# Optimization experiments

Measured on AMD Instinct MI355X. Metric: run time of the kernel, lower is better.

Reference implementation:

```python
import math
import jax, jax.numpy as jnp
import numpy as np

STREAMS = 4
DIM = 1024
M = 16                      # routing granularity
BUS = STREAMS * DIM         # 4096
C = BUS // M                # 256
SINK_ITERS = 10
SINK_TAU = 0.05
B, L = 4, 2048


def rms_norm(x, gamma):
    # F.normalize(x, dim=-1) * sqrt(dim) * (gamma + 1)
    norm = jnp.sqrt(jnp.sum(x * x, axis=-1, keepdims=True))
    x = x / jnp.maximum(norm, 1e-12)
    return x * jnp.sqrt(jnp.asarray(x.shape[-1], x.dtype)) * (gamma + 1.0)


def sinkhorn_log(logits, num_iters=SINK_ITERS, tau=SINK_TAU):
    n = logits.shape[-1]
    Z = logits / tau
    lm = -math.log(n)
    u = jnp.zeros(Z.shape[:-1], Z.dtype)
    v = jnp.zeros(Z.shape[:-2] + (n,), Z.dtype)
    def body(_, uv):
        u, v = uv
        u = lm - jax.nn.logsumexp(Z + v[..., None, :], axis=-1)
        v = lm - jax.nn.logsumexp(Z + u[..., None], axis=-2)
        return (u, v)
    u, v = jax.lax.fori_loop(0, num_iters, body, (u, v))
    return jnp.exp(Z + u[..., None] + v[..., None, :]) * n


def setup_inputs() -> dict:
    key = jax.random.key(0)
    ks = jax.random.split(key, 8)
    residuals = jax.random.normal(ks[0], (B * STREAMS, L, DIM), jnp.float32)
    branch_output = jax.random.normal(ks[1], (B, L, DIM), jnp.float32)
    gamma = jax.random.normal(ks[2], (BUS,), jnp.float32) * 0.02
    H_res_logits = jnp.full((M, M), -8.0, jnp.float32)
    H_res_logits = H_res_logits.at[jnp.arange(M), jnp.arange(M)].set(0.0)
    phi_res = jax.random.normal(ks[3], (BUS, M * M), jnp.float32) * 0.02
    H_pre_logits = jnp.full((STREAMS,), -8.0, jnp.float32).at[0].set(0.0)
    phi_pre = jax.random.normal(ks[4], (BUS, STREAMS), jnp.float32) * 0.02
    H_post_logits = jnp.zeros((STREAMS,), jnp.float32)
    phi_post = jax.random.normal(ks[5], (BUS, STREAMS), jnp.float32) * 0.02
    a = jnp.asarray(0.01, jnp.float32)
    return dict(residuals=residuals, branch_output=branch_output, gamma=gamma,
                H_res_logits=H_res_logits, phi_res=phi_res, alpha_res=a,
                H_pre_logits=H_pre_logits, phi_pre=phi_pre, alpha_pre=a,
                H_post_logits=H_post_logits, phi_post=phi_post, alpha_post=a)


def reference(residuals, branch_output, gamma, H_res_logits, phi_res, alpha_res,
              H_pre_logits, phi_pre, alpha_pre, H_post_logits, phi_post, alpha_post):
    # (b s) l d -> b l s d
    res = residuals.reshape(B, STREAMS, L, DIM).transpose(0, 2, 1, 3)
    bus = res.reshape(B, L, BUS)
    bus_n = rms_norm(bus, gamma)

    raw = (bus_n @ phi_res).reshape(B, L, M, M)
    S = sinkhorn_log(alpha_res * raw + H_res_logits)
    H_res = S  # no identity mix

    H_pre = jax.nn.softmax(alpha_pre * (bus_n @ phi_pre) + H_pre_logits, axis=-1)
    H_post = jax.nn.softmax(alpha_post * (bus_n @ phi_post) + H_post_logits, axis=-1)

    reshaped = res.reshape(B, L, M, C)
    mixed = jnp.einsum('blst,blsc->bltc', H_res, reshaped).reshape(B, L, STREAMS, DIM)

    branch_input = jnp.einsum('bls,blsd->bld', H_pre, res)

    # depth connection with given branch_output
    branch_to_streams = branch_output[..., None, :] * H_post[..., :, None]
    out = mixed + branch_to_streams            # (B, L, STREAMS, DIM)
    out = out.transpose(0, 2, 1, 3).reshape(B * STREAMS, L, DIM)
    return out, branch_input
```

## Files before the change

### kernel.cpp

```cpp
#include <hip/hip_runtime.h>
#include <hip/hip_bf16.h>
#include <math.h>

#define NSTREAM 4
#define DIM     1024
#define BUSW    4096
#define NTOK    8192
#define NPAD    288
#define KSPLIT  4
#define KCH     1024
#define BM      64
#define BK      32
#define OUT0    ((size_t)16 * 2048 * 1024)

typedef short bf16x8 __attribute__((ext_vector_type(8)));
typedef float f32x4  __attribute__((ext_vector_type(4)));

__device__ __forceinline__ unsigned short f2bf(float f) {
    union { float f; unsigned int u; } x; x.f = f;
    unsigned int r = x.u + 0x7fffu + ((x.u >> 16) & 1u);
    return (unsigned short)(r >> 16);
}
__device__ __forceinline__ unsigned int pack2(float a, float b) {
    return (unsigned int)f2bf(a) | ((unsigned int)f2bf(b) << 16);
}

__global__ void prep_w_kernel(const float* __restrict__ gamma,
                              const float* __restrict__ phi_res,
                              const float* __restrict__ phi_pre,
                              const float* __restrict__ phi_post,
                              unsigned short* __restrict__ W) {
    int idx = blockIdx.x * 256 + threadIdx.x;
    int n = idx >> 12;
    int k = idx & 4095;
    float v = 0.0f;
    if (n < 256)      v = phi_res[k * 256 + n];
    else if (n < 260) v = phi_pre[k * 4 + (n - 256)];
    else if (n < 264) v = phi_post[k * 4 + (n - 260)];
    v *= (gamma[k] + 1.0f);
    W[idx] = f2bf(v);
}

__launch_bounds__(256, 2)
__global__ void gemm_raw_kernel(const float* __restrict__ residuals,
                                const unsigned short* __restrict__ W,
                                float* __restrict__ raw_part) {
    __shared__ unsigned short Alds[BM * BK];
    __shared__ unsigned short Blds[NPAD * BK];

    const int tid = threadIdx.x;
    const int wid = tid >> 6, lane = tid & 63;
    const int tb = blockIdx.x, kc = blockIdx.y;
    const int row0 = tb * BM;

    f32x4 acc[2][9];
#pragma unroll
    for (int i = 0; i < 2; i++)
#pragma unroll
        for (int j = 0; j < 9; j++) acc[i][j] = (f32x4){0.f, 0.f, 0.f, 0.f};

    const int arow = tid >> 2;
    const int akq  = (tid & 3) * 8;
    const int tok  = row0 + arow;
    const int bidx = tok >> 11, lidx = tok & 2047;
    const float* abase = residuals +
        (((size_t)(bidx * 4 + kc) * 2048 + lidx) * 1024 + akq);
    const unsigned short* wbase = W + (size_t)kc * KCH;

    const int fr = lane & 15, hf = lane >> 4;
    const int wr = (wid >> 1) * 32;
    const int wc = (wid & 1) * 144;

    for (int kt = 0; kt < KCH / BK; kt++) {
        const float* ap = abase + kt * BK;
        float4 f0 = *(const float4*)(ap);
        float4 f1 = *(const float4*)(ap + 4);
        uint4 ua;
        ua.x = pack2(f0.x, f0.y); ua.y = pack2(f0.z, f0.w);
        ua.z = pack2(f1.x, f1.y); ua.w = pack2(f1.z, f1.w);
        *(uint4*)&Alds[arow * BK + akq] = ua;
#pragma unroll
        for (int i = 0; i < 5; i++) {
            int idx = i * 256 + tid;
            if (idx < (NPAD * BK) / 8) {
                int rn = idx >> 2, ko = (idx & 3) * 8;
                uint4 w = *(const uint4*)(wbase + (size_t)rn * BUSW + kt * BK + ko);
                *(uint4*)&Blds[rn * BK + ko] = w;
            }
        }
        __syncthreads();

        bf16x8 afrag[2], bfrag[9];
#pragma unroll
        for (int mt = 0; mt < 2; mt++)
            afrag[mt] = *(const bf16x8*)&Alds[(wr + mt * 16 + fr) * BK + hf * 8];
#pragma unroll
        for (int nt = 0; nt < 9; nt++)
            bfrag[nt] = *(const bf16x8*)&Blds[(wc + nt * 16 + fr) * BK + hf * 8];
#pragma unroll
        for (int mt = 0; mt < 2; mt++)
#pragma unroll
            for (int nt = 0; nt < 9; nt++)
                acc[mt][nt] = __builtin_amdgcn_mfma_f32_16x16x32_bf16(
                    afrag[mt], bfrag[nt], acc[mt][nt], 0, 0, 0);
        __syncthreads();
    }

#pragma unroll
    for (int mt = 0; mt < 2; mt++)
#pragma unroll
        for (int nt = 0; nt < 9; nt++)
#pragma unroll
            for (int r = 0; r < 4; r++) {
                int token = row0 + wr + mt * 16 + hf * 4 + r;
                int col   = wc + nt * 16 + fr;
                raw_part[((size_t)kc * NTOK + token) * NPAD + col] = acc[mt][nt][r];
            }
}

__global__ void fused_tail_kernel(const float* __restrict__ residuals,
                                  const float* __restrict__ branch_output,
                                  const float* __restrict__ H_res_logits,
                                  const float* __restrict__ alpha_res_p,
                                  const float* __restrict__ H_pre_logits,
                                  const float* __restrict__ alpha_pre_p,
                                  const float* __restrict__ H_post_logits,
                                  const float* __restrict__ alpha_post_p,
                                  const float* __restrict__ raw_part,
                                  float* __restrict__ out) {
    const int t = blockIdx.x;
    const int b = t >> 11, l = t & 2047;
    const int tid = threadIdx.x;
    const int wid = tid >> 6, lane = tid & 63;

    __shared__ float busf[4096];
    __shared__ float Zl[256];
    __shared__ float au[16], bv[16];
    __shared__ float extra[8];
    __shared__ float hpre[4], hpost[4];
    __shared__ float redbuf[4];

    float rsum = 0.f;
#pragma unroll
    for (int kc = 0; kc < 4; kc++)
        rsum += raw_part[((size_t)kc * NTOK + t) * NPAD + tid];
    float esum = 0.f;
    if (tid < 8) {
#pragma unroll
        for (int kc = 0; kc < 4; kc++)
            esum += raw_part[((size_t)kc * NTOK + t) * NPAD + 256 + tid];
    }

    const float* rbase = residuals + ((size_t)b * 4 * 2048 + l) * 1024;
    float sumsq = 0.f;
#pragma unroll
    for (int s = 0; s < 4; s++) {
        float4 v = *(const float4*)(rbase + (size_t)s * 2048 * 1024 + tid * 4);
        *(float4*)&busf[s * 1024 + tid * 4] = v;
        sumsq += v.x * v.x + v.y * v.y + v.z * v.z + v.w * v.w;
    }
#pragma unroll
    for (int off = 32; off > 0; off >>= 1) sumsq += __shfl_down(sumsq, off, 64);
    if (lane == 0) redbuf[wid] = sumsq;
    __syncthreads();

    const float ss = redbuf[0] + redbuf[1] + redbuf[2] + redbuf[3];
    const float scale = 64.0f / fmaxf(sqrtf(ss), 1e-12f);

    const float a_res = alpha_res_p[0];
    Zl[tid] = __expf((a_res * scale * rsum + H_res_logits[tid]) * 20.0f);
    if (tid < 8) extra[tid] = esum;

    const float* bo = branch_output + ((size_t)b * 2048 + l) * 1024;
    float bor[4];
#pragma unroll
    for (int j = 0; j < 4; j++) bor[j] = bo[j * 256 + tid];

    __syncthreads();

    if (wid == 0) {
        const float c0 = 1.0f / 16.0f;
        const bool act = lane < 16;
        const int r = lane & 15;
        if (act) bv[r] = 1.0f;
        __builtin_amdgcn_sched_barrier(0);
        float a_own = 0.f;
        for (int it = 0; it < 10; it++) {
            if (act) {
                float s2 = 0.f;
#pragma unroll
                for (int c = 0; c < 16; c++) s2 += Zl[r * 16 + c] * bv[c];
                a_own = c0 / s2;
                au[r] = a_own;
            }
            __builtin_amdgcn_sched_barrier(0);
            if (act) {
                float s2 = 0.f;
#pragma unroll
                for (int rr = 0; rr < 16; rr++) s2 += Zl[rr * 16 + r] * au[rr];
                bv[r] = c0 / s2;
            }
            __builtin_amdgcn_sched_barrier(0);
        }
        if (act) {
#pragma unroll
            for (int c = 0; c < 16; c++)
                Zl[r * 16 + c] = 16.0f * Zl[r * 16 + c] * a_own * bv[c];
        }
    } else if (wid == 1) {
        if (lane < 8) {
            const int s = lane & 3;
            const bool pre = lane < 4;
            const float alpha = pre ? alpha_pre_p[0] : alpha_post_p[0];
            const float logit = pre ? H_pre_logits[s] : H_post_logits[s];
            float pv = alpha * scale * extra[pre ? s : 4 + s] + logit;
            float pm = fmaxf(pv, __shfl_xor(pv, 1, 4));
            pm = fmaxf(pm, __shfl_xor(pm, 2, 4));
            float e = __expf(pv - pm);
            float s2 = e + __shfl_xor(e, 1, 4);
            s2 += __shfl_xor(s2, 2, 4);
            float h = e / s2;
            if (pre) hpre[s] = h; else hpost[s] = h;
        }
    }
    __syncthreads();

    float busr[16];
#pragma unroll
    for (int s = 0; s < 16; s++) busr[s] = busf[s * 256 + tid];
#pragma unroll
    for (int tc = 0; tc < 16; tc++) {
        float acc2 = 0.f;
#pragma unroll
        for (int s = 0; s < 16; s++) acc2 += Zl[s * 16 + tc] * busr[s];
        int sout = tc >> 2, d = (tc & 3) * 256 + tid;
        float val = acc2 + bor[tc & 3] * hpost[sout];
        out[((size_t)(b * 4 + sout) * 2048 + l) * 1024 + d] = val;
    }

    int d0 = tid * 4;
    float4 bi; bi.x = bi.y = bi.z = bi.w = 0.f;
#pragma unroll
    for (int s = 0; s < 4; s++) {
        float4 v = *(const float4*)&busf[s * 1024 + d0];
        float h = hpre[s];
        bi.x += h * v.x; bi.y += h * v.y; bi.z += h * v.z; bi.w += h * v.w;
    }
    *(float4*)&out[OUT0 + ((size_t)b * 2048 + l) * 1024 + d0] = bi;
}

extern "C" void kernel_launch(void* const* d_in, const int* in_sizes, int n_in,
                              void* d_out, int out_size, void* d_ws, size_t ws_size,
                              hipStream_t stream) {
    const float* residuals  = (const float*)d_in[0];
    const float* branch_out = (const float*)d_in[1];
    const float* gamma      = (const float*)d_in[2];
    const float* H_res_log  = (const float*)d_in[3];
    const float* phi_res    = (const float*)d_in[4];
    const float* alpha_res  = (const float*)d_in[5];
    const float* H_pre_log  = (const float*)d_in[6];
    const float* phi_pre    = (const float*)d_in[7];
    const float* alpha_pre  = (const float*)d_in[8];
    const float* H_post_log = (const float*)d_in[9];
    const float* phi_post   = (const float*)d_in[10];
    const float* alpha_post = (const float*)d_in[11];

    unsigned short* W = (unsigned short*)d_ws;
    float* raw_part = (float*)((char*)d_ws + (size_t)NPAD * BUSW * 2);
    float* out = (float*)d_out;

    hipLaunchKernelGGL(prep_w_kernel, dim3(NPAD * BUSW / 256), dim3(256), 0, stream,
                       gamma, phi_res, phi_pre, phi_post, W);
    hipLaunchKernelGGL(gemm_raw_kernel, dim3(NTOK / BM, KSPLIT), dim3(256), 0, stream,
                       residuals, W, raw_part);
    hipLaunchKernelGGL(fused_tail_kernel, dim3(NTOK), dim3(256), 0, stream,
                       residuals, branch_out, H_res_log, alpha_res,
                       H_pre_log, alpha_pre, H_post_log, alpha_post, raw_part, out);
}
```

Baseline: 400.0 us.

## Use direct global-to-LDS loads for W and keep bus rows in registers

The GEMM now stages W tiles with global_load_lds, which bypasses VGPRs, and interleaves B-fragment loads with MFMAs. It also raises the launch-bounds occupancy hint from 2 to 4 blocks per CU. The tail kernel drops the 16KB shared bus buffer and keeps each thread's 16 residual values in registers using coalesced scalar loads, which should raise tail occupancy and remove LDS traffic. The cost is more register pressure under the tighter launch bounds and scalar rather than float4 global accesses.

```diff
diff --git a/kernel.cpp b/kernel.cpp
--- a/kernel.cpp
+++ b/kernel.cpp
@@ -23,6 +23,12 @@
 }
 __device__ __forceinline__ unsigned int pack2(float a, float b) {
     return (unsigned int)f2bf(a) | ((unsigned int)f2bf(b) << 16);
+}
+
+__device__ __forceinline__ void gload_lds16(const void* g, void* l) {
+    __builtin_amdgcn_global_load_lds(
+        (const __attribute__((address_space(1))) unsigned int*)g,
+        (__attribute__((address_space(3))) unsigned int*)l, 16, 0, 0);
 }
 
 __global__ void prep_w_kernel(const float* __restrict__ gamma,
@@ -41,12 +47,12 @@
     W[idx] = f2bf(v);
 }
 
-__launch_bounds__(256, 2)
+__launch_bounds__(256, 4)
 __global__ void gemm_raw_kernel(const float* __restrict__ residuals,
                                 const unsigned short* __restrict__ W,
                                 float* __restrict__ raw_part) {
-    __shared__ unsigned short Alds[BM * BK];
-    __shared__ unsigned short Blds[NPAD * BK];
+    __shared__ __align__(16) unsigned short Alds[BM * BK];
+    __shared__ __align__(16) unsigned short Blds[NPAD * BK];
 
     const int tid = threadIdx.x;
     const int wid = tid >> 6, lane = tid & 63;
@@ -65,13 +71,23 @@
     const int bidx = tok >> 11, lidx = tok & 2047;
     const float* abase = residuals +
         (((size_t)(bidx * 4 + kc) * 2048 + lidx) * 1024 + akq);
-    const unsigned short* wbase = W + (size_t)kc * KCH;
+    const char* wbytes = (const char*)(W + (size_t)kc * KCH);
 
     const int fr = lane & 15, hf = lane >> 4;
     const int wr = (wid >> 1) * 32;
     const int wc = (wid & 1) * 144;
 
     for (int kt = 0; kt < KCH / BK; kt++) {
+#pragma unroll
+        for (int i = 0; i < 5; i++) {
+            int idx = i * 256 + tid;
+            if (idx < (NPAD * BK) / 8) {
+                int rn = idx >> 2;
+                const void* g = wbytes + (size_t)rn * (BUSW * 2) + kt * (BK * 2)
+                                + (idx & 3) * 16;
+                gload_lds16(g, (char*)Blds + idx * 16);
+            }
+        }
         const float* ap = abase + kt * BK;
         float4 f0 = *(const float4*)(ap);
         float4 f1 = *(const float4*)(ap + 4);
@@ -79,30 +95,20 @@
         ua.x = pack2(f0.x, f0.y); ua.y = pack2(f0.z, f0.w);
         ua.z = pack2(f1.x, f1.y); ua.w = pack2(f1.z, f1.w);
         *(uint4*)&Alds[arow * BK + akq] = ua;
-#pragma unroll
-        for (int i = 0; i < 5; i++) {
-            int idx = i * 256 + tid;
-            if (idx < (NPAD * BK) / 8) {
-                int rn = idx >> 2, ko = (idx & 3) * 8;
-                uint4 w = *(const uint4*)(wbase + (size_t)rn * BUSW + kt * BK + ko);
-                *(uint4*)&Blds[rn * BK + ko] = w;
-            }
-        }
         __syncthreads();
 
-        bf16x8 afrag[2], bfrag[9];
+        bf16x8 afrag[2];
 #pragma unroll
         for (int mt = 0; mt < 2; mt++)
             afrag[mt] = *(const bf16x8*)&Alds[(wr + mt * 16 + fr) * BK + hf * 8];
 #pragma unroll
-        for (int nt = 0; nt < 9; nt++)
-            bfrag[nt] = *(const bf16x8*)&Blds[(wc + nt * 16 + fr) * BK + hf * 8];
-#pragma unroll
-        for (int mt = 0; mt < 2; mt++)
-#pragma unroll
-            for (int nt = 0; nt < 9; nt++)
-                acc[mt][nt] = __builtin_amdgcn_mfma_f32_16x16x32_bf16(
-                    afrag[mt], bfrag[nt], acc[mt][nt], 0, 0, 0);
+        for (int nt = 0; nt < 9; nt++) {
+            bf16x8 bfrag = *(const bf16x8*)&Blds[(wc + nt * 16 + fr) * BK + hf * 8];
+            acc[0][nt] = __builtin_amdgcn_mfma_f32_16x16x32_bf16(
+                afrag[0], bfrag, acc[0][nt], 0, 0, 0);
+            acc[1][nt] = __builtin_amdgcn_mfma_f32_16x16x32_bf16(
+                afrag[1], bfrag, acc[1][nt], 0, 0, 0);
+        }
         __syncthreads();
     }
 
@@ -133,7 +139,6 @@
     const int tid = threadIdx.x;
     const int wid = tid >> 6, lane = tid & 63;
 
-    __shared__ float busf[4096];
     __shared__ float Zl[256];
     __shared__ float au[16], bv[16];
     __shared__ float extra[8];
@@ -152,12 +157,12 @@
     }
 
     const float* rbase = residuals + ((size_t)b * 4 * 2048 + l) * 1024;
+    float busr[16];
     float sumsq = 0.f;
 #pragma unroll
-    for (int s = 0; s < 4; s++) {
-        float4 v = *(const float4*)(rbase + (size_t)s * 2048 * 1024 + tid * 4);
-        *(float4*)&busf[s * 1024 + tid * 4] = v;
-        sumsq += v.x * v.x + v.y * v.y + v.z * v.z + v.w * v.w;
+    for (int j = 0; j < 16; j++) {
+        busr[j] = rbase[(size_t)(j >> 2) * 2048 * 1024 + (j & 3) * 256 + tid];
+        sumsq += busr[j] * busr[j];
     }
 #pragma unroll
     for (int off = 32; off > 0; off >>= 1) sumsq += __shfl_down(sumsq, off, 64);
@@ -225,9 +230,6 @@
     }
     __syncthreads();
 
-    float busr[16];
-#pragma unroll
-    for (int s = 0; s < 16; s++) busr[s] = busf[s * 256 + tid];
 #pragma unroll
     for (int tc = 0; tc < 16; tc++) {
         float acc2 = 0.f;
@@ -238,15 +240,13 @@
         out[((size_t)(b * 4 + sout) * 2048 + l) * 1024 + d] = val;
     }
 
-    int d0 = tid * 4;
-    float4 bi; bi.x = bi.y = bi.z = bi.w = 0.f;
-#pragma unroll
-    for (int s = 0; s < 4; s++) {
-        float4 v = *(const float4*)&busf[s * 1024 + d0];
-        float h = hpre[s];
-        bi.x += h * v.x; bi.y += h * v.y; bi.z += h * v.z; bi.w += h * v.w;
-    }
-    *(float4*)&out[OUT0 + ((size_t)b * 2048 + l) * 1024 + d0] = bi;
+#pragma unroll
+    for (int q = 0; q < 4; q++) {
+        float bi = 0.f;
+#pragma unroll
+        for (int s = 0; s < 4; s++) bi += hpre[s] * busr[s * 4 + q];
+        out[OUT0 + ((size_t)b * 2048 + l) * 1024 + q * 256 + tid] = bi;
+    }
 }
 
 extern "C" void kernel_launch(void* const* d_in, const int* in_sizes, int n_in,
```

Measured after the change: 383.2 us. -4.2%, faster.
